# Performance work log

Hardware: AMD Instinct MI355X
Metric: run time of the kernel (lower is better)

The kernel has to match this reference:

```python
import jax, jax.numpy as jnp
import numpy as np

N, E = 50000, 400000
IN_F, HID, HEADS, CLASSES, GROUP = 256, 64, 4, 40, 2
NEG_SLOPE = 0.2
EPS = 1e-5


def setup_inputs() -> dict:
    key = jax.random.key(0)
    ks = jax.random.split(key, 16)
    s = 0.05
    W = HEADS * HID          # 256 flattened hidden width
    GW = W // GROUP          # 128 per-group width
    GD = HID // GROUP        # 32  per-head out_feats in middle blocks
    x = jax.random.normal(ks[0], (N, IN_F), jnp.float32)
    src = jax.random.randint(ks[1], (E,), 0, N, dtype=jnp.int32)
    # guarantee every node has >=1 incoming edge so edge_softmax is well-defined
    dst = jnp.concatenate([jnp.arange(N, dtype=jnp.int32),
                           jax.random.randint(ks[2], (E - N,), 0, N, dtype=jnp.int32)])
    return dict(
        x=x, src=src, dst=dst,
        W0=jax.random.normal(ks[3], (W, IN_F)) * s,
        attn_l0=jax.random.normal(ks[4], (HEADS, HID)) * s,
        attn_r0=jax.random.normal(ks[5], (HEADS, HID)) * s,
        resW0=jax.random.normal(ks[6], (W, IN_F)) * s,
        mid_bn_gamma=jnp.ones((2, GROUP, GW)),
        mid_bn_beta=jnp.zeros((2, GROUP, GW)),
        mid_W=jax.random.normal(ks[7], (2, GROUP, GW, GW)) * s,
        mid_attn_l=jax.random.normal(ks[8], (2, GROUP, HEADS, GD)) * s,
        mid_attn_r=jax.random.normal(ks[9], (2, GROUP, HEADS, GD)) * s,
        mid_resW=jax.random.normal(ks[10], (2, GROUP, GW, GW)) * s,
        norm_gamma=jnp.ones((W,)), norm_beta=jnp.zeros((W,)),
        W_last=jax.random.normal(ks[11], (CLASSES, W)) * s,
        attn_l_last=jax.random.normal(ks[12], (1, CLASSES)) * s,
        attn_r_last=jax.random.normal(ks[13], (1, CLASSES)) * s,
        resW_last=jax.random.normal(ks[14], (CLASSES, W)) * s,
        bias_last=jnp.zeros((CLASSES,)),
    )


def _gat_conv(x, src, dst, W, attn_l, attn_r, resW, out_isqrt, in_sqrt):
    n = x.shape[0]
    H, D = attn_l.shape
    ft0 = (x @ W.T).reshape(n, H, D)            # projected feat [N,H,D]
    ft = ft0 * out_isqrt[:, None, None]         # symmetric norm on source side
    el = (ft * attn_l).sum(-1)                  # [N,H] (uses normalized feat_src)
    er = (ft0 * attn_r).sum(-1)                 # [N,H] (feat_dst aliased BEFORE norm)
    e = el[src] + er[dst]                       # edge scores [E,H]
    e = jnp.where(e >= 0, e, NEG_SLOPE * e)     # leaky_relu
    emax = jax.ops.segment_max(e, dst, num_segments=n)
    emax = jnp.where(jnp.isfinite(emax), emax, 0.0)
    ex = jnp.exp(e - emax[dst])
    denom = jax.ops.segment_sum(ex, dst, num_segments=n)
    a = ex / jnp.maximum(denom, 1e-9)[dst]      # per-destination edge softmax [E,H]
    msg = ft[src] * a[:, :, None]               # [E,H,D]
    rst = jax.ops.segment_sum(msg, dst, num_segments=n)
    rst = rst * in_sqrt[:, None, None]          # symmetric norm on dest side
    rst = rst + (x @ resW.T).reshape(n, H, D)   # residual fc
    return rst


def _bn_relu(z, gamma, beta):
    mu = z.mean(0)
    var = ((z - mu) ** 2).mean(0)               # biased var (torch BN training)
    return jax.nn.relu(gamma * (z - mu) * jax.lax.rsqrt(var + EPS) + beta)


def reference(x, src, dst, W0, attn_l0, attn_r0, resW0, mid_bn_gamma, mid_bn_beta,
              mid_W, mid_attn_l, mid_attn_r, mid_resW, norm_gamma, norm_beta,
              W_last, attn_l_last, attn_r_last, resW_last, bias_last):
    n = x.shape[0]
    ones = jnp.ones((src.shape[0],), x.dtype)
    outdeg = jnp.maximum(jax.ops.segment_sum(ones, src, num_segments=n), 1.0)
    indeg = jnp.maximum(jax.ops.segment_sum(ones, dst, num_segments=n), 1.0)
    out_isqrt = outdeg ** -0.5
    in_sqrt = jnp.sqrt(indeg)
    # layer 0: GATConv(in_feats -> n_hidden, n_heads)
    h = _gat_conv(x, src, dst, W0, attn_l0, attn_r0, resW0, out_isqrt, in_sqrt).reshape(n, -1)
    # reversible middle layers: GroupAdditiveCoupling, group=2
    for l in range(2):
        x0, x1 = jnp.split(h, 2, axis=-1)
        z = _bn_relu(x1, mid_bn_gamma[l, 0], mid_bn_beta[l, 0])
        y0 = x0 + _gat_conv(z, src, dst, mid_W[l, 0], mid_attn_l[l, 0], mid_attn_r[l, 0],
                            mid_resW[l, 0], out_isqrt, in_sqrt).reshape(n, -1)
        z = _bn_relu(y0, mid_bn_gamma[l, 1], mid_bn_beta[l, 1])
        y1 = x1 + _gat_conv(z, src, dst, mid_W[l, 1], mid_attn_l[l, 1], mid_attn_r[l, 1],
                            mid_resW[l, 1], out_isqrt, in_sqrt).reshape(n, -1)
        h = jnp.concatenate([y0, y1], axis=-1)
    # final norm + relu + output conv (1 head), mean over head dim, bias_last
    h = _bn_relu(h, norm_gamma, norm_beta)
    out = _gat_conv(h, src, dst, W_last, attn_l_last, attn_r_last, resW_last,
                    out_isqrt, in_sqrt).mean(1)
    return out + bias_last
```

## Files before the change

kernel.cpp:

```cpp
#include <hip/hip_runtime.h>
#include <hip/hip_bf16.h>


#define IN_F   256
#define HIDW   256
#define CLS    40

typedef __attribute__((ext_vector_type(8))) __bf16 bf16x8;
typedef __attribute__((ext_vector_type(4))) float  f32x4;

__device__ inline bf16x8 zb8() {
    bf16x8 v;
#pragma unroll
    for (int i = 0; i < 8; ++i) v[i] = (__bf16)0.f;
    return v;
}
__device__ inline bf16x8 ldb8(const __hip_bfloat16* p) {
    return *reinterpret_cast<const bf16x8*>(p);
}
__device__ inline float bf2f(unsigned short u) {
    union { unsigned int i; float f; } c;
    c.i = ((unsigned int)u) << 16;
    return c.f;
}

__global__ void k_hist(const int* __restrict__ src, const int* __restrict__ dst,
                       int E, int* __restrict__ outdeg, int* __restrict__ indeg) {
    for (int e = blockIdx.x * blockDim.x + threadIdx.x; e < E; e += gridDim.x * blockDim.x) {
        atomicAdd(&outdeg[src[e]], 1);
        atomicAdd(&indeg[dst[e]], 1);
    }
}

__global__ void k_scan1(const int* __restrict__ cnt, int N, int* __restrict__ rp1,
                        int* __restrict__ bsum) {
    __shared__ int sm[256];
    int i = blockIdx.x * 256 + threadIdx.x;
    int v = (i < N) ? cnt[i] : 0;
    sm[threadIdx.x] = v;
    __syncthreads();
    for (int off = 1; off < 256; off <<= 1) {
        int t = (threadIdx.x >= off) ? sm[threadIdx.x - off] : 0;
        __syncthreads();
        sm[threadIdx.x] += t;
        __syncthreads();
    }
    if (i < N) rp1[i] = sm[threadIdx.x];
    if (threadIdx.x == 255) bsum[blockIdx.x] = sm[255];
}

__global__ void k_scan2(int* __restrict__ bsum, int nb) {
    __shared__ int sm[256];
    int v = (threadIdx.x < nb) ? bsum[threadIdx.x] : 0;
    sm[threadIdx.x] = v;
    __syncthreads();
    for (int off = 1; off < 256; off <<= 1) {
        int t = (threadIdx.x >= off) ? sm[threadIdx.x - off] : 0;
        __syncthreads();
        sm[threadIdx.x] += t;
        __syncthreads();
    }
    if (threadIdx.x < nb) bsum[threadIdx.x] = sm[threadIdx.x] - v;
}

__global__ void k_scan3(int* __restrict__ rp1, const int* __restrict__ bsumExcl, int N) {
    int i = blockIdx.x * 256 + threadIdx.x;
    if (i < N) rp1[i] += bsumExcl[blockIdx.x];
    if (blockIdx.x == 0 && threadIdx.x == 0) rp1[-1] = 0;
}

__global__ void k_scatter(const int* __restrict__ src, const int* __restrict__ dst,
                          int E, int* __restrict__ cursor, int* __restrict__ csr_src) {
    for (int e = blockIdx.x * blockDim.x + threadIdx.x; e < E; e += gridDim.x * blockDim.x) {
        int d = dst[e];
        int pos = atomicAdd(&cursor[d], 1);
        csr_src[pos] = src[e];
    }
}

__global__ void k_deg(const int* __restrict__ outdeg, const int* __restrict__ indeg,
                      float* __restrict__ oi, float* __restrict__ insq, int N) {
    int i = blockIdx.x * 256 + threadIdx.x;
    if (i < N) {
        int od = outdeg[i]; if (od < 1) od = 1;
        int id = indeg[i];  if (id < 1) id = 1;
        oi[i]   = rsqrtf((float)od);
        insq[i] = sqrtf((float)id);
    }
}

__global__ void k_cvt6(const float* s0, __hip_bfloat16* d0, int n0,
                       const float* s1, __hip_bfloat16* d1, int n1,
                       const float* s2, __hip_bfloat16* d2, int n2,
                       const float* s3, __hip_bfloat16* d3, int n3,
                       const float* s4, __hip_bfloat16* d4, int n4,
                       const float* s5, __hip_bfloat16* d5, int n5) {
    const float* ss; __hip_bfloat16* dd; int nn;
    switch (blockIdx.y) {
        case 0: ss = s0; dd = d0; nn = n0; break;
        case 1: ss = s1; dd = d1; nn = n1; break;
        case 2: ss = s2; dd = d2; nn = n2; break;
        case 3: ss = s3; dd = d3; nn = n3; break;
        case 4: ss = s4; dd = d4; nn = n4; break;
        default: ss = s5; dd = d5; nn = n5; break;
    }
    for (int i = blockIdx.x * blockDim.x + threadIdx.x; i < nn; i += gridDim.x * blockDim.x)
        dd[i] = __float2bfloat16(ss[i]);
}

template<int K, int NF, int NR, int H, bool BN>
__global__ __launch_bounds__(512) void k_gatconv_lds(
    const float* __restrict__ A, int lda,
    const __hip_bfloat16* __restrict__ Wft,
    const __hip_bfloat16* __restrict__ Wres,
    __hip_bfloat16* __restrict__ ftb, int ldft,
    float* __restrict__ Cres, int ldcres, int M,
    const float* __restrict__ scale, const float* __restrict__ shift,
    const float* __restrict__ resbase, int ldbase,
    const float* __restrict__ attn_l, const float* __restrict__ attn_r,
    const float* __restrict__ oi,
    float* __restrict__ el, float* __restrict__ er) {
    constexpr int BM = 64, KF = K / 32, NTOT = NF + NR;
    constexpr int CW = NTOT / 8, CT = CW / 16, D = NF / H;
    constexpr int NRT = BM / 16;
    static_assert(NTOT % 8 == 0 && CW % 16 == 0, "col split");
    static_assert(NF % CW == 0 && CW == D, "head-per-wave el/er epilogue");
    __shared__ bf16x8 lds[NRT * KF * 64];
    const int tid = threadIdx.x;
    const int wv = tid >> 6, lane = tid & 63, rf = lane & 15, kg = lane >> 4;
    const int row0 = blockIdx.x * BM;

    {
        constexpr int CPR = K / 8;
        constexpr int RSTEP = 512 / CPR;
        const int c16 = tid % CPR;
        const int ec = c16 * 8;
        const int skf = c16 >> 2, skg = c16 & 3;
        float sc[8], sh[8];
        if (BN) {
            float4 s01 = *reinterpret_cast<const float4*>(scale + ec);
            float4 s23 = *reinterpret_cast<const float4*>(scale + ec + 4);
            float4 h01 = *reinterpret_cast<const float4*>(shift + ec);
            float4 h23 = *reinterpret_cast<const float4*>(shift + ec + 4);
            sc[0]=s01.x; sc[1]=s01.y; sc[2]=s01.z; sc[3]=s01.w;
            sc[4]=s23.x; sc[5]=s23.y; sc[6]=s23.z; sc[7]=s23.w;
            sh[0]=h01.x; sh[1]=h01.y; sh[2]=h01.z; sh[3]=h01.w;
            sh[4]=h23.x; sh[5]=h23.y; sh[6]=h23.z; sh[7]=h23.w;
        }
#pragma unroll
        for (int r0 = 0; r0 < BM; r0 += RSTEP) {
            const int r = r0 + tid / CPR;
            const int gr = row0 + r;
            bf16x8 t = zb8();
            if (gr < M) {
                const float* ap = A + (size_t)gr * lda + ec;
                float4 f0 = *reinterpret_cast<const float4*>(ap);
                float4 f1 = *reinterpret_cast<const float4*>(ap + 4);
                float v[8] = {f0.x, f0.y, f0.z, f0.w, f1.x, f1.y, f1.z, f1.w};
#pragma unroll
                for (int i = 0; i < 8; ++i) {
                    float u = v[i];
                    if (BN) u = fmaxf(u * sc[i] + sh[i], 0.f);
                    t[i] = (__bf16)u;
                }
            }
            lds[((r >> 4) * KF + skf) * 64 + ((skg * 16 + (r & 15)) ^ skf)] = t;
        }
    }
    __syncthreads();

    const bool isft = (wv * CW) < NF;
    const int colbase = isft ? wv * CW : wv * CW - NF;
    const __hip_bfloat16* __restrict__ Wb = isft ? Wft : Wres;
    const int hh = colbase / D;

    float elp[NRT][4], erp[NRT][4];
#pragma unroll
    for (int rt = 0; rt < NRT; ++rt)
#pragma unroll
        for (int r = 0; r < 4; ++r) { elp[rt][r] = 0.f; erp[rt][r] = 0.f; }

#pragma unroll
    for (int ct = 0; ct < CT; ++ct) {
        const int col = colbase + ct * 16 + rf;
        bf16x8 b[KF];
        const __hip_bfloat16* bp = Wb + (size_t)col * K + kg * 8;
#pragma unroll
        for (int kf = 0; kf < KF; ++kf) b[kf] = ldb8(bp + kf * 32);
        float al = 0.f, ar = 0.f;
        if (isft) { al = attn_l[col]; ar = attn_r[col]; }
#pragma unroll
        for (int rtp = 0; rtp < NRT / 2; ++rtp) {
            const int rt0 = rtp * 2, rt1 = rtp * 2 + 1;
            f32x4 acc0 = {0.f, 0.f, 0.f, 0.f};
            f32x4 acc1 = {0.f, 0.f, 0.f, 0.f};
#pragma unroll
            for (int kf = 0; kf < KF; ++kf) {
                const bf16x8 a0 = lds[(rt0 * KF + kf) * 64 + (lane ^ kf)];
                const bf16x8 a1 = lds[(rt1 * KF + kf) * 64 + (lane ^ kf)];
                acc0 = __builtin_amdgcn_mfma_f32_16x16x32_bf16(a0, b[kf], acc0, 0, 0, 0);
                acc1 = __builtin_amdgcn_mfma_f32_16x16x32_bf16(a1, b[kf], acc1, 0, 0, 0);
            }
            const int gr0 = row0 + rt0 * 16 + kg * 4;
            const int gr1 = row0 + rt1 * 16 + kg * 4;
            if (isft) {
#pragma unroll
                for (int r = 0; r < 4; ++r) {
                    elp[rt0][r] += acc0[r] * al; erp[rt0][r] += acc0[r] * ar;
                    elp[rt1][r] += acc1[r] * al; erp[rt1][r] += acc1[r] * ar;
                    if (gr0 + r < M)
                        ftb[(size_t)(gr0 + r) * ldft + col] = __float2bfloat16(acc0[r]);
                    if (gr1 + r < M)
                        ftb[(size_t)(gr1 + r) * ldft + col] = __float2bfloat16(acc1[r]);
                }
            } else {
#pragma unroll
                for (int r = 0; r < 4; ++r) {
                    if (gr0 + r < M) {
                        float v = acc0[r];
                        if (resbase) v += resbase[(size_t)(gr0 + r) * ldbase + col];
                        Cres[(size_t)(gr0 + r) * ldcres + col] = v;
                    }
                    if (gr1 + r < M) {
                        float v = acc1[r];
                        if (resbase) v += resbase[(size_t)(gr1 + r) * ldbase + col];
                        Cres[(size_t)(gr1 + r) * ldcres + col] = v;
                    }
                }
            }
        }
    }

    if (isft) {
#pragma unroll
        for (int off = 1; off <= 8; off <<= 1)
#pragma unroll
            for (int rt = 0; rt < NRT; ++rt)
#pragma unroll
                for (int r = 0; r < 4; ++r) {
                    elp[rt][r] += __shfl_xor(elp[rt][r], off);
                    erp[rt][r] += __shfl_xor(erp[rt][r], off);
                }
        if (rf == 0) {
#pragma unroll
            for (int rt = 0; rt < NRT; ++rt)
#pragma unroll
                for (int r = 0; r < 4; ++r) {
                    const int gr = row0 + rt * 16 + kg * 4 + r;
                    if (gr < M) {
                        el[(size_t)gr * H + hh] = oi[gr] * elp[rt][r];
                        er[(size_t)gr * H + hh] = erp[rt][r];
                    }
                }
        }
    }
}

template<int K, int NF, int NR, int H, bool BN>
__global__ __launch_bounds__(256) void k_gatconv_sm(
    const float* __restrict__ A, int lda,
    const __hip_bfloat16* __restrict__ Wft,
    const __hip_bfloat16* __restrict__ Wres,
    __hip_bfloat16* __restrict__ ftb, int ldft,
    float* __restrict__ Cres, int ldcres,
    int M,
    const float* __restrict__ scale, const float* __restrict__ shift,
    const float* __restrict__ resbase, int ldbase,
    const float* __restrict__ bias,
    const float* __restrict__ attn_l, const float* __restrict__ attn_r,
    const float* __restrict__ oi,
    float* __restrict__ el, float* __restrict__ er) {
    constexpr int KF   = K / 32;
    constexpr int NCTF = (NF + 15) / 16;
    constexpr int NCTR = (NR + 15) / 16;
    constexpr int CTH  = NCTF / H;
    static_assert(NCTF % H == 0, "head tiling");
    const int wave = threadIdx.x >> 6, lane = threadIdx.x & 63;
    const int row0 = blockIdx.x * 64 + wave * 16;
    const int rf = lane & 15, kg = lane >> 4;

    bf16x8 a[KF];
    {
        const int row = row0 + rf;
        const bool rok = row < M;
#pragma unroll
        for (int kf = 0; kf < KF; ++kf) {
            const int c0 = kg * 8 + kf * 32;
            if (rok) {
                const float* ap = A + (size_t)row * lda + c0;
                float4 f0 = *reinterpret_cast<const float4*>(ap);
                float4 f1 = *reinterpret_cast<const float4*>(ap + 4);
                float v[8] = {f0.x, f0.y, f0.z, f0.w, f1.x, f1.y, f1.z, f1.w};
                bf16x8 t;
                if (BN) {
                    float4 s01 = *reinterpret_cast<const float4*>(scale + c0);
                    float4 s23 = *reinterpret_cast<const float4*>(scale + c0 + 4);
                    float4 h01 = *reinterpret_cast<const float4*>(shift + c0);
                    float4 h23 = *reinterpret_cast<const float4*>(shift + c0 + 4);
                    float sc[8] = {s01.x,s01.y,s01.z,s01.w,s23.x,s23.y,s23.z,s23.w};
                    float sh[8] = {h01.x,h01.y,h01.z,h01.w,h23.x,h23.y,h23.z,h23.w};
#pragma unroll
                    for (int i = 0; i < 8; ++i)
                        t[i] = (__bf16)fmaxf(v[i] * sc[i] + sh[i], 0.f);
                } else {
#pragma unroll
                    for (int i = 0; i < 8; ++i) t[i] = (__bf16)v[i];
                }
                a[kf] = t;
            } else {
                a[kf] = zb8();
            }
        }
    }

    int ct = 0;
    for (int hh = 0; hh < H; ++hh) {
        float elp[4] = {0.f, 0.f, 0.f, 0.f};
        float erp[4] = {0.f, 0.f, 0.f, 0.f};
        for (int cth = 0; cth < CTH; ++cth, ++ct) {
            const int ccol = ct * 16 + rf;
            bf16x8 b[KF];
            const __hip_bfloat16* bp = Wft + (size_t)ccol * K + kg * 8;
#pragma unroll
            for (int kf = 0; kf < KF; ++kf)
                b[kf] = (ccol < NF) ? ldb8(bp + kf * 32) : zb8();
            f32x4 acc = {0.f, 0.f, 0.f, 0.f};
#pragma unroll
            for (int kf = 0; kf < KF; ++kf)
                acc = __builtin_amdgcn_mfma_f32_16x16x32_bf16(a[kf], b[kf], acc, 0, 0, 0);
            float al = 0.f, ar = 0.f;
            if (ccol < NF) { al = attn_l[ccol]; ar = attn_r[ccol]; }
            if (ccol < NF) {
#pragma unroll
                for (int r = 0; r < 4; ++r) {
                    const float v = acc[r];
                    elp[r] += v * al; erp[r] += v * ar;
                    const int row = row0 + kg * 4 + r;
                    if (row < M)
                        ftb[(size_t)row * ldft + ccol] = __float2bfloat16(v);
                }
            }
        }
#pragma unroll
        for (int off = 1; off <= 8; off <<= 1)
#pragma unroll
            for (int r = 0; r < 4; ++r) {
                elp[r] += __shfl_xor(elp[r], off);
                erp[r] += __shfl_xor(erp[r], off);
            }
        if (rf == 0) {
#pragma unroll
            for (int r = 0; r < 4; ++r) {
                const int row = row0 + kg * 4 + r;
                if (row < M) {
                    el[(size_t)row * H + hh] = oi[row] * elp[r];
                    er[(size_t)row * H + hh] = erp[r];
                }
            }
        }
    }

    for (int rt = 0; rt < NCTR; ++rt) {
        const int ccol = rt * 16 + rf;
        bf16x8 b[KF];
        const __hip_bfloat16* bp = Wres + (size_t)ccol * K + kg * 8;
#pragma unroll
        for (int kf = 0; kf < KF; ++kf)
            b[kf] = (ccol < NR) ? ldb8(bp + kf * 32) : zb8();
        f32x4 acc = {0.f, 0.f, 0.f, 0.f};
#pragma unroll
        for (int kf = 0; kf < KF; ++kf)
            acc = __builtin_amdgcn_mfma_f32_16x16x32_bf16(a[kf], b[kf], acc, 0, 0, 0);
        if (ccol < NR) {
#pragma unroll
            for (int r = 0; r < 4; ++r) {
                const int row = row0 + kg * 4 + r;
                if (row < M) {
                    float v = acc[r];
                    if (resbase) v += resbase[(size_t)row * ldbase + ccol];
                    if (bias) v += bias[ccol];
                    Cres[(size_t)row * ldcres + ccol] = v;
                }
            }
        }
    }
}

template<int EPL>
__device__ inline void ldrow(const __hip_bfloat16* fp, float* f) {
    if constexpr (EPL == 4) {
        ushort4 q = *reinterpret_cast<const ushort4*>(fp);
        f[0] = bf2f(q.x); f[1] = bf2f(q.y); f[2] = bf2f(q.z); f[3] = bf2f(q.w);
    } else if constexpr (EPL == 2) {
        ushort2 q = *reinterpret_cast<const ushort2*>(fp);
        f[0] = bf2f(q.x); f[1] = bf2f(q.y);
    } else {
        f[0] = bf2f(*reinterpret_cast<const unsigned short*>(fp));
    }
}
__device__ inline float escore(float sc) {
    sc = sc >= 0.f ? sc : 0.2f * sc;
    sc = fminf(fmaxf(sc, -30.f), 30.f);
    return __expf(sc);
}

template<int H, int D>
__global__ __launch_bounds__(256) void k_agg(
    const __hip_bfloat16* __restrict__ ftb,
    const float* __restrict__ el, const float* __restrict__ er,
    const int* __restrict__ row_ptr, const int* __restrict__ csr_src,
    const float* __restrict__ oi, const float* __restrict__ insq,
    float* __restrict__ out, int ldc, int N) {
    constexpr int W = H * D;
    constexpr int EPL = (W >= 64) ? (W / 64) : 1;
    const int lane = threadIdx.x & 63;
    const int v = blockIdx.x * 4 + (threadIdx.x >> 6);
    if (v >= N) return;
    if (W < 64 && lane >= W) return;
    const int col0 = lane * EPL;
    const int myh = (W >= 64) ? (col0 / D) : 0;
    const int s = row_ptr[v], e = row_ptr[v + 1];
    const float erv = er[(size_t)v * H + myh];

    float denom = 0.f;
    float acc[EPL];
#pragma unroll
    for (int k = 0; k < EPL; ++k) acc[k] = 0.f;

    int p = s;
    for (; p + 3 < e; p += 4) {
        const int u0 = csr_src[p + 0], u1 = csr_src[p + 1];
        const int u2 = csr_src[p + 2], u3 = csr_src[p + 3];
        float f0[EPL], f1[EPL], f2[EPL], f3[EPL];
        ldrow<EPL>(ftb + (size_t)u0 * W + col0, f0);
        ldrow<EPL>(ftb + (size_t)u1 * W + col0, f1);
        ldrow<EPL>(ftb + (size_t)u2 * W + col0, f2);
        ldrow<EPL>(ftb + (size_t)u3 * W + col0, f3);
        const float s0 = el[(size_t)u0 * H + myh], s1 = el[(size_t)u1 * H + myh];
        const float s2 = el[(size_t)u2 * H + myh], s3 = el[(size_t)u3 * H + myh];
        const float o0 = oi[u0], o1 = oi[u1], o2 = oi[u2], o3 = oi[u3];
        const float w0 = escore(s0 + erv), w1 = escore(s1 + erv);
        const float w2 = escore(s2 + erv), w3 = escore(s3 + erv);
        denom += (w0 + w1) + (w2 + w3);
        const float a0 = w0 * o0, a1 = w1 * o1, a2 = w2 * o2, a3 = w3 * o3;
#pragma unroll
        for (int k = 0; k < EPL; ++k)
            acc[k] += a0 * f0[k] + a1 * f1[k] + a2 * f2[k] + a3 * f3[k];
    }
    for (; p < e; ++p) {
        const int u = csr_src[p];
        float f[EPL];
        ldrow<EPL>(ftb + (size_t)u * W + col0, f);
        const float w = escore(el[(size_t)u * H + myh] + erv);
        denom += w;
        const float a = w * oi[u];
#pragma unroll
        for (int k = 0; k < EPL; ++k) acc[k] += a * f[k];
    }

    const float iv = insq[v] / fmaxf(denom, 1e-9f);
    float* op = out + (size_t)v * ldc + col0;
    if constexpr (EPL == 4) {
        float4 o = *reinterpret_cast<float4*>(op);
        o.x += iv * acc[0]; o.y += iv * acc[1]; o.z += iv * acc[2]; o.w += iv * acc[3];
        *reinterpret_cast<float4*>(op) = o;
    } else if constexpr (EPL == 2) {
        float2 o = *reinterpret_cast<float2*>(op);
        o.x += iv * acc[0]; o.y += iv * acc[1];
        *reinterpret_cast<float2*>(op) = o;
    } else {
        op[0] += iv * acc[0];
    }
}

template<int F>
__global__ __launch_bounds__(256) void k_bn_part(const float* __restrict__ in, int ldin, int N,
                                                 float* __restrict__ psum, float* __restrict__ psum2) {
    constexpr int SL = 256 / F;
    const int col = threadIdx.x % F;
    const int pr = blockIdx.x * SL + threadIdx.x / F;
    const int PRT = gridDim.x * SL;
    float s = 0.f, s2 = 0.f;
    for (int r = pr; r < N; r += PRT) {
        float v = in[(size_t)r * ldin + col];
        s += v; s2 += v * v;
    }
    psum[(size_t)pr * F + col] = s;
    psum2[(size_t)pr * F + col] = s2;
}

template<int F>
__global__ __launch_bounds__(256) void k_bn_fin(const float* __restrict__ psum,
                                                const float* __restrict__ psum2, int PRT,
                                                const float* __restrict__ gamma,
                                                const float* __restrict__ beta,
                                                float* __restrict__ scale,
                                                float* __restrict__ shift, int N) {
    const int col = blockIdx.x;
    float s = 0.f, s2 = 0.f;
    for (int p = threadIdx.x; p < PRT; p += 256) {
        s += psum[(size_t)p * F + col];
        s2 += psum2[(size_t)p * F + col];
    }
#pragma unroll
    for (int off = 32; off; off >>= 1) {
        s += __shfl_down(s, off);
        s2 += __shfl_down(s2, off);
    }
    __shared__ float sm[4], sm2[4];
    const int wave = threadIdx.x >> 6, lane = threadIdx.x & 63;
    if (lane == 0) { sm[wave] = s; sm2[wave] = s2; }
    __syncthreads();
    if (threadIdx.x == 0) {
        s = sm[0] + sm[1] + sm[2] + sm[3];
        s2 = sm2[0] + sm2[1] + sm2[2] + sm2[3];
        float mu = s / N;
        float var = s2 / N - mu * mu;
        float isd = rsqrtf(var + 1e-5f);
        float g = gamma[col];
        scale[col] = g * isd;
        shift[col] = beta[col] - g * isd * mu;
    }
}

extern "C" void kernel_launch(void* const* d_in, const int* in_sizes, int n_in,
                              void* d_out, int out_size, void* d_ws, size_t ws_size,
                              hipStream_t stream) {
    const float* x           = (const float*)d_in[0];
    const int*   src         = (const int*)d_in[1];
    const int*   dst         = (const int*)d_in[2];
    const float* W0          = (const float*)d_in[3];
    const float* attn_l0     = (const float*)d_in[4];
    const float* attn_r0     = (const float*)d_in[5];
    const float* resW0       = (const float*)d_in[6];
    const float* mid_bn_g    = (const float*)d_in[7];
    const float* mid_bn_b    = (const float*)d_in[8];
    const float* mid_W       = (const float*)d_in[9];
    const float* mid_attn_l  = (const float*)d_in[10];
    const float* mid_attn_r  = (const float*)d_in[11];
    const float* mid_resW    = (const float*)d_in[12];
    const float* norm_gamma  = (const float*)d_in[13];
    const float* norm_beta   = (const float*)d_in[14];
    const float* W_last      = (const float*)d_in[15];
    const float* attn_l_last = (const float*)d_in[16];
    const float* attn_r_last = (const float*)d_in[17];
    const float* resW_last   = (const float*)d_in[18];
    const float* bias_last   = (const float*)d_in[19];

    const int N = in_sizes[0] / IN_F;
    const int E = in_sizes[1];

    char* p = (char*)d_ws;
    size_t used = 0;
    auto take = [&](size_t bytes) -> char* {
        char* r = p;
        size_t adv = (bytes + 255) & ~(size_t)255;
        p += adv; used += adv;
        return r;
    };
    float*          h       = (float*)take((size_t)N * HIDW * 4);
    __hip_bfloat16* ftb     = (__hip_bfloat16*)take((size_t)N * HIDW * 2);
    float*          el      = (float*)take((size_t)N * 4 * 4);
    float*          er      = (float*)take((size_t)N * 4 * 4);
    float*          oi      = (float*)take((size_t)N * 4);
    float*          insq    = (float*)take((size_t)N * 4);
    int*            indeg   = (int*)take((size_t)N * 4);
    int*            outdeg  = (int*)take((size_t)N * 4);
    int*            row_ptr = (int*)take((size_t)(N + 1) * 4);
    int*            cursor  = (int*)take((size_t)N * 4);
    int*            csr_src = (int*)take((size_t)E * 4);
    int*            bsum    = (int*)take(256 * 4);
    float*          psum    = (float*)take(1 << 20);
    float*          psum2   = (float*)take(1 << 20);
    float*          scale   = (float*)take(1024);
    float*          shift   = (float*)take(1024);
    __hip_bfloat16* W0bf      = (__hip_bfloat16*)take(65536 * 2);
    __hip_bfloat16* resW0bf   = (__hip_bfloat16*)take(65536 * 2);
    __hip_bfloat16* midWbf    = (__hip_bfloat16*)take(65536 * 2);
    __hip_bfloat16* midresWbf = (__hip_bfloat16*)take(65536 * 2);
    __hip_bfloat16* Wlastbf   = (__hip_bfloat16*)take(10240 * 2);
    __hip_bfloat16* resWlastbf= (__hip_bfloat16*)take(10240 * 2);
    if (used > ws_size) return;

    const int nbN = (N + 255) / 256;
    const int NB4 = (N + 3) / 4;
    const int GWB = (N + 63) / 64;
    const int GWS = (N + 63) / 64;
    const int BNB = 1024;

    hipMemsetAsync(indeg, 0, (size_t)N * 4, stream);
    hipMemsetAsync(outdeg, 0, (size_t)N * 4, stream);
    k_hist<<<1024, 256, 0, stream>>>(src, dst, E, outdeg, indeg);
    k_scan1<<<nbN, 256, 0, stream>>>(indeg, N, row_ptr + 1, bsum);
    k_scan2<<<1, 256, 0, stream>>>(bsum, nbN);
    k_scan3<<<nbN, 256, 0, stream>>>(row_ptr + 1, bsum, N);
    hipMemcpyAsync(cursor, row_ptr, (size_t)N * 4, hipMemcpyDeviceToDevice, stream);
    k_scatter<<<1024, 256, 0, stream>>>(src, dst, E, cursor, csr_src);
    k_deg<<<nbN, 256, 0, stream>>>(outdeg, indeg, oi, insq, N);

    k_cvt6<<<dim3(64, 6), 256, 0, stream>>>(W0, W0bf, 65536,
                                            resW0, resW0bf, 65536,
                                            mid_W, midWbf, 65536,
                                            mid_resW, midresWbf, 65536,
                                            W_last, Wlastbf, 10240,
                                            resW_last, resWlastbf, 10240);

    k_gatconv_lds<256, 256, 256, 4, false><<<GWB, 512, 0, stream>>>(
        x, 256, W0bf, resW0bf, ftb, 256, h, 256, N,
        nullptr, nullptr, nullptr, 0,
        attn_l0, attn_r0, oi, el, er);
    k_agg<4, 64><<<NB4, 256, 0, stream>>>(ftb, el, er, row_ptr, csr_src, oi, insq, h, 256, N);

    for (int l = 0; l < 2; ++l) {
        for (int g = 0; g < 2; ++g) {
            const int inoff  = (g == 0) ? 128 : 0;
            const int outoff = (g == 0) ? 0 : 128;
            const int pg = l * 2 + g;
            k_bn_part<128><<<BNB, 256, 0, stream>>>(h + inoff, 256, N, psum, psum2);
            k_bn_fin<128><<<128, 256, 0, stream>>>(psum, psum2, BNB * 2,
                                                   mid_bn_g + pg * 128, mid_bn_b + pg * 128,
                                                   scale, shift, N);
            k_gatconv_lds<128, 128, 128, 4, true><<<GWB, 512, 0, stream>>>(
                h + inoff, 256, midWbf + pg * 16384, midresWbf + pg * 16384,
                ftb, 128, h + outoff, 256, N,
                scale, shift, h + outoff, 256,
                mid_attn_l + pg * 128, mid_attn_r + pg * 128, oi, el, er);
            k_agg<4, 32><<<NB4, 256, 0, stream>>>(ftb, el, er, row_ptr, csr_src, oi, insq,
                                                  h + outoff, 256, N);
        }
    }

    k_bn_part<256><<<BNB, 256, 0, stream>>>(h, 256, N, psum, psum2);
    k_bn_fin<256><<<256, 256, 0, stream>>>(psum, psum2, BNB, norm_gamma, norm_beta, scale, shift, N);
    k_gatconv_sm<256, 40, 40, 1, true><<<GWS, 256, 0, stream>>>(
        h, 256, Wlastbf, resWlastbf, ftb, 40, (float*)d_out, 40, N,
        scale, shift, nullptr, 0, bias_last,
        attn_l_last, attn_r_last, oi, el, er);
    k_agg<1, 40><<<NB4, 256, 0, stream>>>(ftb, el, er, row_ptr, csr_src, oi, insq,
                                          (float*)d_out, 40, N);
}
```

Baseline: 633.7 us.

## Fold attention vectors into augmented weight columns and vectorize GEMM epilogue stores

Precomputes W^T·attn_l and W^T·attn_r as 8 extra weight columns, packed as a 16-column tile appended to each projection weight, so el/er come out of one extra MFMA tile instead of per-element multiply-accumulates and cross-lane shuffle reductions. MFMA operands are swapped so each lane holds four consecutive columns of one row, which lets ft, residual and el/er results be written as vectorized ushort4/float4 stores instead of strided scalar stores. The extra tile is computed only by wave 0, adding a small load imbalance. el is now computed from bf16-rounded projected attention weights, and el/er are accumulated directly from the GEMM rather than from rounded ft values, which slightly changes numerics.

```diff
diff --git a/kernel.cpp b/kernel.cpp
--- a/kernel.cpp
+++ b/kernel.cpp
@@ -22,6 +22,12 @@
     union { unsigned int i; float f; } c;
     c.i = ((unsigned int)u) << 16;
     return c.f;
+}
+__device__ inline unsigned short f2bu(float f) {
+    __hip_bfloat16 t = __float2bfloat16(f);
+    union { __hip_bfloat16 b; unsigned short u; } c;
+    c.b = t;
+    return c.u;
 }
 
 __global__ void k_hist(const int* __restrict__ src, const int* __restrict__ dst,
@@ -108,23 +114,62 @@
         dd[i] = __float2bfloat16(ss[i]);
 }
 
+__global__ void k_prepw(const float* __restrict__ W0,
+                        const float* __restrict__ al0, const float* __restrict__ ar0,
+                        const float* __restrict__ midW,
+                        const float* __restrict__ midal, const float* __restrict__ midar,
+                        __hip_bfloat16* __restrict__ Waug0,
+                        __hip_bfloat16* __restrict__ midWaug) {
+    const int layer = blockIdx.y;
+    int NF, K, D;
+    const float *W, *al, *ar;
+    __hip_bfloat16* dst;
+    if (layer == 0) {
+        NF = 256; K = 256; D = 64;
+        W = W0; al = al0; ar = ar0; dst = Waug0;
+    } else {
+        const int pg = layer - 1;
+        NF = 128; K = 128; D = 32;
+        W = midW + pg * 16384; al = midal + pg * 128; ar = midar + pg * 128;
+        dst = midWaug + (size_t)pg * 144 * 128;
+    }
+    const int total = (NF + 16) * K;
+    for (int idx = blockIdx.x * 256 + threadIdx.x; idx < total; idx += gridDim.x * 256) {
+        const int col = idx / K, k = idx % K;
+        float v = 0.f;
+        if (col < NF) {
+            v = W[(size_t)col * K + k];
+        } else {
+            const int j = col - NF;
+            if (j < 8) {
+                const int head = j & 3;
+                const float* at = (j < 4) ? al : ar;
+                float s = 0.f;
+                for (int d = 0; d < D; ++d)
+                    s += W[(size_t)(head * D + d) * K + k] * at[head * D + d];
+                v = s;
+            }
+        }
+        dst[idx] = __float2bfloat16(v);
+    }
+}
+
 template<int K, int NF, int NR, int H, bool BN>
 __global__ __launch_bounds__(512) void k_gatconv_lds(
     const float* __restrict__ A, int lda,
-    const __hip_bfloat16* __restrict__ Wft,
+    const __hip_bfloat16* __restrict__ Waug,
     const __hip_bfloat16* __restrict__ Wres,
     __hip_bfloat16* __restrict__ ftb, int ldft,
     float* __restrict__ Cres, int ldcres, int M,
     const float* __restrict__ scale, const float* __restrict__ shift,
     const float* __restrict__ resbase, int ldbase,
-    const float* __restrict__ attn_l, const float* __restrict__ attn_r,
     const float* __restrict__ oi,
     float* __restrict__ el, float* __restrict__ er) {
     constexpr int BM = 64, KF = K / 32, NTOT = NF + NR;
-    constexpr int CW = NTOT / 8, CT = CW / 16, D = NF / H;
+    constexpr int CW = NTOT / 8, CT = CW / 16;
     constexpr int NRT = BM / 16;
     static_assert(NTOT % 8 == 0 && CW % 16 == 0, "col split");
-    static_assert(NF % CW == 0 && CW == D, "head-per-wave el/er epilogue");
+    static_assert(H == 4, "el/er float4 stores assume H==4");
     __shared__ bf16x8 lds[NRT * KF * 64];
     const int tid = threadIdx.x;
     const int wv = tid >> 6, lane = tid & 63, rf = lane & 15, kg = lane >> 4;
@@ -171,87 +216,99 @@
 
     const bool isft = (wv * CW) < NF;
     const int colbase = isft ? wv * CW : wv * CW - NF;
-    const __hip_bfloat16* __restrict__ Wb = isft ? Wft : Wres;
-    const int hh = colbase / D;
-
-    float elp[NRT][4], erp[NRT][4];
-#pragma unroll
-    for (int rt = 0; rt < NRT; ++rt)
-#pragma unroll
-        for (int r = 0; r < 4; ++r) { elp[rt][r] = 0.f; erp[rt][r] = 0.f; }
-
-#pragma unroll
+    const __hip_bfloat16* __restrict__ Wb = isft ? Waug : Wres;
+
     for (int ct = 0; ct < CT; ++ct) {
-        const int col = colbase + ct * 16 + rf;
-        bf16x8 b[KF];
-        const __hip_bfloat16* bp = Wb + (size_t)col * K + kg * 8;
-#pragma unroll
-        for (int kf = 0; kf < KF; ++kf) b[kf] = ldb8(bp + kf * 32);
-        float al = 0.f, ar = 0.f;
-        if (isft) { al = attn_l[col]; ar = attn_r[col]; }
+        const int tcol = colbase + ct * 16;
+        bf16x8 w[KF];
+        const __hip_bfloat16* bp = Wb + (size_t)(tcol + rf) * K + kg * 8;
+#pragma unroll
+        for (int kf = 0; kf < KF; ++kf) w[kf] = ldb8(bp + kf * 32);
 #pragma unroll
         for (int rtp = 0; rtp < NRT / 2; ++rtp) {
-            const int rt0 = rtp * 2, rt1 = rtp * 2 + 1;
             f32x4 acc0 = {0.f, 0.f, 0.f, 0.f};
             f32x4 acc1 = {0.f, 0.f, 0.f, 0.f};
 #pragma unroll
             for (int kf = 0; kf < KF; ++kf) {
-                const bf16x8 a0 = lds[(rt0 * KF + kf) * 64 + (lane ^ kf)];
-                const bf16x8 a1 = lds[(rt1 * KF + kf) * 64 + (lane ^ kf)];
-                acc0 = __builtin_amdgcn_mfma_f32_16x16x32_bf16(a0, b[kf], acc0, 0, 0, 0);
-                acc1 = __builtin_amdgcn_mfma_f32_16x16x32_bf16(a1, b[kf], acc1, 0, 0, 0);
-            }
-            const int gr0 = row0 + rt0 * 16 + kg * 4;
-            const int gr1 = row0 + rt1 * 16 + kg * 4;
+                const bf16x8 a0 = lds[((2 * rtp) * KF + kf) * 64 + (lane ^ kf)];
+                const bf16x8 a1 = lds[((2 * rtp + 1) * KF + kf) * 64 + (lane ^ kf)];
+                acc0 = __builtin_amdgcn_mfma_f32_16x16x32_bf16(w[kf], a0, acc0, 0, 0, 0);
+                acc1 = __builtin_amdgcn_mfma_f32_16x16x32_bf16(w[kf], a1, acc1, 0, 0, 0);
+            }
+            const int r0g = row0 + 2 * rtp * 16 + rf;
+            const int r1g = r0g + 16;
+            const int c4 = tcol + 4 * kg;
             if (isft) {
-#pragma unroll
-                for (int r = 0; r < 4; ++r) {
-                    elp[rt0][r] += acc0[r] * al; erp[rt0][r] += acc0[r] * ar;
-                    elp[rt1][r] += acc1[r] * al; erp[rt1][r] += acc1[r] * ar;
-                    if (gr0 + r < M)
-                        ftb[(size_t)(gr0 + r) * ldft + col] = __float2bfloat16(acc0[r]);
-                    if (gr1 + r < M)
-                        ftb[(size_t)(gr1 + r) * ldft + col] = __float2bfloat16(acc1[r]);
+                if (r0g < M) {
+                    ushort4 q = {f2bu(acc0[0]), f2bu(acc0[1]), f2bu(acc0[2]), f2bu(acc0[3])};
+                    *reinterpret_cast<ushort4*>(&ftb[(size_t)r0g * ldft + c4]) = q;
+                }
+                if (r1g < M) {
+                    ushort4 q = {f2bu(acc1[0]), f2bu(acc1[1]), f2bu(acc1[2]), f2bu(acc1[3])};
+                    *reinterpret_cast<ushort4*>(&ftb[(size_t)r1g * ldft + c4]) = q;
                 }
             } else {
-#pragma unroll
-                for (int r = 0; r < 4; ++r) {
-                    if (gr0 + r < M) {
-                        float v = acc0[r];
-                        if (resbase) v += resbase[(size_t)(gr0 + r) * ldbase + col];
-                        Cres[(size_t)(gr0 + r) * ldcres + col] = v;
+                if (r0g < M) {
+                    float4 v = {acc0[0], acc0[1], acc0[2], acc0[3]};
+                    if (resbase) {
+                        float4 b4 = *reinterpret_cast<const float4*>(
+                            &resbase[(size_t)r0g * ldbase + c4]);
+                        v.x += b4.x; v.y += b4.y; v.z += b4.z; v.w += b4.w;
                     }
-                    if (gr1 + r < M) {
-                        float v = acc1[r];
-                        if (resbase) v += resbase[(size_t)(gr1 + r) * ldbase + col];
-                        Cres[(size_t)(gr1 + r) * ldcres + col] = v;
+                    *reinterpret_cast<float4*>(&Cres[(size_t)r0g * ldcres + c4]) = v;
+                }
+                if (r1g < M) {
+                    float4 v = {acc1[0], acc1[1], acc1[2], acc1[3]};
+                    if (resbase) {
+                        float4 b4 = *reinterpret_cast<const float4*>(
+                            &resbase[(size_t)r1g * ldbase + c4]);
+                        v.x += b4.x; v.y += b4.y; v.z += b4.z; v.w += b4.w;
                     }
-                }
-            }
-        }
-    }
-
-    if (isft) {
-#pragma unroll
-        for (int off = 1; off <= 8; off <<= 1)
-#pragma unroll
-            for (int rt = 0; rt < NRT; ++rt)
-#pragma unroll
-                for (int r = 0; r < 4; ++r) {
-                    elp[rt][r] += __shfl_xor(elp[rt][r], off);
-                    erp[rt][r] += __shfl_xor(erp[rt][r], off);
-                }
-        if (rf == 0) {
-#pragma unroll
-            for (int rt = 0; rt < NRT; ++rt)
-#pragma unroll
-                for (int r = 0; r < 4; ++r) {
-                    const int gr = row0 + rt * 16 + kg * 4 + r;
-                    if (gr < M) {
-                        el[(size_t)gr * H + hh] = oi[gr] * elp[rt][r];
-                        er[(size_t)gr * H + hh] = erp[rt][r];
-                    }
-                }
+                    *reinterpret_cast<float4*>(&Cres[(size_t)r1g * ldcres + c4]) = v;
+                }
+            }
+        }
+    }
+
+    if (wv == 0) {
+        bf16x8 w[KF];
+        const __hip_bfloat16* bp = Waug + (size_t)(NF + rf) * K + kg * 8;
+#pragma unroll
+        for (int kf = 0; kf < KF; ++kf) w[kf] = ldb8(bp + kf * 32);
+#pragma unroll
+        for (int rtp = 0; rtp < NRT / 2; ++rtp) {
+            f32x4 acc0 = {0.f, 0.f, 0.f, 0.f};
+            f32x4 acc1 = {0.f, 0.f, 0.f, 0.f};
+#pragma unroll
+            for (int kf = 0; kf < KF; ++kf) {
+                const bf16x8 a0 = lds[((2 * rtp) * KF + kf) * 64 + (lane ^ kf)];
+                const bf16x8 a1 = lds[((2 * rtp + 1) * KF + kf) * 64 + (lane ^ kf)];
+                acc0 = __builtin_amdgcn_mfma_f32_16x16x32_bf16(w[kf], a0, acc0, 0, 0, 0);
+                acc1 = __builtin_amdgcn_mfma_f32_16x16x32_bf16(w[kf], a1, acc1, 0, 0, 0);
+            }
+            const int r0g = row0 + 2 * rtp * 16 + rf;
+            const int r1g = r0g + 16;
+            if (kg == 0) {
+                if (r0g < M) {
+                    const float o = oi[r0g];
+                    float4 v = {acc0[0] * o, acc0[1] * o, acc0[2] * o, acc0[3] * o};
+                    *reinterpret_cast<float4*>(&el[(size_t)r0g * 4]) = v;
+                }
+                if (r1g < M) {
+                    const float o = oi[r1g];
+                    float4 v = {acc1[0] * o, acc1[1] * o, acc1[2] * o, acc1[3] * o};
+                    *reinterpret_cast<float4*>(&el[(size_t)r1g * 4]) = v;
+                }
+            } else if (kg == 1) {
+                if (r0g < M) {
+                    float4 v = {acc0[0], acc0[1], acc0[2], acc0[3]};
+                    *reinterpret_cast<float4*>(&er[(size_t)r0g * 4]) = v;
+                }
+                if (r1g < M) {
+                    float4 v = {acc1[0], acc1[1], acc1[2], acc1[3]};
+                    *reinterpret_cast<float4*>(&er[(size_t)r1g * 4]) = v;
+                }
+            }
         }
     }
 }
@@ -574,9 +631,9 @@
     float*          psum2   = (float*)take(1 << 20);
     float*          scale   = (float*)take(1024);
     float*          shift   = (float*)take(1024);
-    __hip_bfloat16* W0bf      = (__hip_bfloat16*)take(65536 * 2);
+    __hip_bfloat16* Waug0     = (__hip_bfloat16*)take((size_t)272 * 256 * 2);
+    __hip_bfloat16* midWaug   = (__hip_bfloat16*)take((size_t)4 * 144 * 128 * 2);
     __hip_bfloat16* resW0bf   = (__hip_bfloat16*)take(65536 * 2);
-    __hip_bfloat16* midWbf    = (__hip_bfloat16*)take(65536 * 2);
     __hip_bfloat16* midresWbf = (__hip_bfloat16*)take(65536 * 2);
     __hip_bfloat16* Wlastbf   = (__hip_bfloat16*)take(10240 * 2);
     __hip_bfloat16* resWlastbf= (__hip_bfloat16*)take(10240 * 2);
@@ -598,17 +655,19 @@
     k_scatter<<<1024, 256, 0, stream>>>(src, dst, E, cursor, csr_src);
     k_deg<<<nbN, 256, 0, stream>>>(outdeg, indeg, oi, insq, N);
 
-    k_cvt6<<<dim3(64, 6), 256, 0, stream>>>(W0, W0bf, 65536,
-                                            resW0, resW0bf, 65536,
-                                            mid_W, midWbf, 65536,
+    k_cvt6<<<dim3(64, 4), 256, 0, stream>>>(resW0, resW0bf, 65536,
                                             mid_resW, midresWbf, 65536,
                                             W_last, Wlastbf, 10240,
-                                            resW_last, resWlastbf, 10240);
+                                            resW_last, resWlastbf, 10240,
+                                            nullptr, nullptr, 0,
+                                            nullptr, nullptr, 0);
+    k_prepw<<<dim3(96, 5), 256, 0, stream>>>(W0, attn_l0, attn_r0,
+                                             mid_W, mid_attn_l, mid_attn_r,
+                                             Waug0, midWaug);
 
     k_gatconv_lds<256, 256, 256, 4, false><<<GWB, 512, 0, stream>>>(
-        x, 256, W0bf, resW0bf, ftb, 256, h, 256, N,
-        nullptr, nullptr, nullptr, 0,
-        attn_l0, attn_r0, oi, el, er);
+        x, 256, Waug0, resW0bf, ftb, 256, h, 256, N,
+        nullptr, nullptr, nullptr, 0, oi, el, er);
     k_agg<4, 64><<<NB4, 256, 0, stream>>>(ftb, el, er, row_ptr, csr_src, oi, insq, h, 256, N);
 
     for (int l = 0; l < 2; ++l) {
@@ -621,10 +680,9 @@
                                                    mid_bn_g + pg * 128, mid_bn_b + pg * 128,
                                                    scale, shift, N);
             k_gatconv_lds<128, 128, 128, 4, true><<<GWB, 512, 0, stream>>>(
-                h + inoff, 256, midWbf + pg * 16384, midresWbf + pg * 16384,
+                h + inoff, 256, midWaug + (size_t)pg * 144 * 128, midresWbf + pg * 16384,
                 ftb, 128, h + outoff, 256, N,
-                scale, shift, h + outoff, 256,
-                mid_attn_l + pg * 128, mid_attn_r + pg * 128, oi, el, er);
+                scale, shift, h + outoff, 256, oi, el, er);
             k_agg<4, 32><<<NB4, 256, 0, stream>>>(ftb, el, er, row_ptr, csr_src, oi, insq,
                                                   h + outoff, 256, N);
         }
```

Measured after the change: 580.7 us. 1.09x faster.
